# Kernel optimization log

Measured on AMD Instinct MI355X. Metric: run time of the kernel, lower is better.

## Reference

```python
import jax, jax.numpy as jnp
import numpy as np

N_NODES = 50000
N_EDGES = 800000
IN_CH = 128
HIDDEN = [128, 128]
OUT_CH = 64


def _glorot(key, shape):
    fan_in, fan_out = shape
    lim = (6.0 / (fan_in + fan_out)) ** 0.5
    return jax.random.uniform(key, shape, jnp.float32, -lim, lim)


def setup_inputs() -> dict:
    key = jax.random.key(0)
    ks = jax.random.split(key, 12)
    x = jax.random.normal(ks[0], (N_NODES, IN_CH), jnp.float32)
    edge_index = jax.random.randint(ks[1], (2, N_EDGES), 0, N_NODES, jnp.int64)
    dims = [IN_CH] + HIDDEN + [OUT_CH]
    params = {}
    for i in range(len(dims) - 1):
        d_in, d_out = dims[i], dims[i + 1]
        params[f"W_l{i}"] = _glorot(ks[2 + 3 * i], (d_in, d_out))      # neighbor weight
        params[f"W_r{i}"] = _glorot(ks[3 + 3 * i], (d_in, d_out))      # root/self weight
        params[f"b{i}"] = jnp.zeros((d_out,), jnp.float32)
    return {"x": x, "edge_index": edge_index, **params}


def _sage_conv(x, src, dst, W_l, W_r, b):
    # mean-aggregate neighbor features: messages flow src -> dst
    n = x.shape[0]
    agg = jax.ops.segment_sum(x[src], dst, num_segments=n)            # [N, d_in]
    cnt = jax.ops.segment_sum(jnp.ones((src.shape[0],), x.dtype), dst, num_segments=n)
    mean = agg / jnp.maximum(cnt, 1.0)[:, None]
    # PyG SAGEConv: lin_l(mean_neighbors) + lin_r(x_self); bias on lin_l only
    return mean @ W_l + x @ W_r + b


def reference(x, edge_index,
              W_l0, W_r0, b0,
              W_l1, W_r1, b1,
              W_l2, W_r2, b2):
    src, dst = edge_index[0], edge_index[1]
    h = _sage_conv(x, src, dst, W_l0, W_r0, b0)
    h = jax.nn.elu(h)
    h = _sage_conv(h, src, dst, W_l1, W_r1, b1)
    h = jax.nn.elu(h)
    out = _sage_conv(h, src, dst, W_l2, W_r2, b2)
    return out
```

## Files before the change

kernel.cpp:

```cpp
#include <hip/hip_runtime.h>
#include <math.h>

#define N_NODES 50000
#define N_EDGES 800000
#define IN_CH 128
#define NBUCK 196
#define BCAP 5120
#define EPB 4082

typedef unsigned short ushort_t;
typedef unsigned int uint_t;
typedef __attribute__((ext_vector_type(8))) short bf16x8;
typedef __attribute__((ext_vector_type(4))) float f32x4;

static __device__ __forceinline__ ushort_t f32_to_bf16(float f) {
    uint_t u = __float_as_uint(f);
    uint_t r = (u + 0x7fffu + ((u >> 16) & 1u)) >> 16;
    return (ushort_t)r;
}

static __device__ __forceinline__ void acc8(float* a, uint4 v) {
    a[0] += __uint_as_float(v.x << 16); a[1] += __uint_as_float(v.x & 0xffff0000u);
    a[2] += __uint_as_float(v.y << 16); a[3] += __uint_as_float(v.y & 0xffff0000u);
    a[4] += __uint_as_float(v.z << 16); a[5] += __uint_as_float(v.z & 0xffff0000u);
    a[6] += __uint_as_float(v.w << 16); a[7] += __uint_as_float(v.w & 0xffff0000u);
}

__global__ __launch_bounds__(256) void binA(
    const int* __restrict__ src, const int* __restrict__ dst,
    uint_t* __restrict__ gbcnt, uint_t* __restrict__ gbuck) {
    __shared__ uint_t hist[NBUCK];
    __shared__ uint_t excl_s[NBUCK];
    __shared__ uint_t gbase[NBUCK];
    __shared__ uint_t cur[NBUCK];
    __shared__ uint_t pfx[256];
    __shared__ uint_t stage[4096];
    __shared__ uint_t gpos[4096];
    const int t = threadIdx.x;
    const int e0 = blockIdx.x * EPB;
    const int e1 = min(e0 + EPB, N_EDGES);

    for (int i = t; i < NBUCK; i += 256) hist[i] = 0;
    __syncthreads();
    for (int e = e0 + t; e < e1; e += 256) atomicAdd(&hist[dst[e] >> 8], 1u);
    __syncthreads();
    uint_t own = (t < NBUCK) ? hist[t] : 0;
    pfx[t] = own;
    __syncthreads();
    for (int d = 1; d < 256; d <<= 1) {
        uint_t v = (t >= d) ? pfx[t - d] : 0;
        __syncthreads();
        pfx[t] += v;
        __syncthreads();
    }
    if (t < NBUCK) {
        uint_t excl = pfx[t] - own;
        excl_s[t] = excl;
        cur[t] = excl;
        gbase[t] = atomicAdd(&gbcnt[t], own);
    }
    __syncthreads();
    for (int e = e0 + t; e < e1; e += 256) {
        int d_ = dst[e];
        int b = d_ >> 8;
        uint_t p = atomicAdd(&cur[b], 1u);
        stage[p] = ((uint_t)(d_ & 255) << 16) | (uint_t)src[e];
        gpos[p] = (uint_t)b * BCAP + gbase[b] + (p - excl_s[b]);
    }
    __syncthreads();
    const int n = e1 - e0;
    for (int i = t; i < n; i += 256) gbuck[gpos[i]] = stage[i];
}

__global__ __launch_bounds__(256) void binB(
    const uint_t* __restrict__ gbcnt, const uint_t* __restrict__ gbuck,
    int* __restrict__ offs, int* __restrict__ ebuf) {
    __shared__ uint_t pairs[BCAP];
    __shared__ int stage[BCAP];
    __shared__ uint_t bscan[256];
    __shared__ uint_t h[256];
    __shared__ uint_t psc[256];
    __shared__ int cur[256];
    const int b = blockIdx.x;
    const int t = threadIdx.x;

    uint_t g = (t < NBUCK) ? gbcnt[t] : 0;
    bscan[t] = g;
    __syncthreads();
    for (int d = 1; d < 256; d <<= 1) {
        uint_t v = (t >= d) ? bscan[t - d] : 0;
        __syncthreads();
        bscan[t] += v;
        __syncthreads();
    }
    const int base = (b > 0) ? (int)bscan[b - 1] : 0;
    const uint_t n = gbcnt[b];

    for (uint_t i = t; i < n; i += 256) pairs[i] = gbuck[(size_t)b * BCAP + i];
    h[t] = 0;
    __syncthreads();
    for (uint_t i = t; i < n; i += 256) atomicAdd(&h[(pairs[i] >> 16) & 255u], 1u);
    __syncthreads();
    uint_t own = h[t];
    psc[t] = own;
    __syncthreads();
    for (int d = 1; d < 256; d <<= 1) {
        uint_t v = (t >= d) ? psc[t - d] : 0;
        __syncthreads();
        psc[t] += v;
        __syncthreads();
    }
    const int excl = (int)(psc[t] - own);
    const int node = b * 256 + t;
    if (node <= N_NODES) offs[node] = base + excl;
    cur[t] = excl;
    __syncthreads();
    for (uint_t i = t; i < n; i += 256) {
        uint_t p = pairs[i];
        int l = (p >> 16) & 255;
        int pos = atomicAdd(&cur[l], 1);
        stage[pos] = (int)(p & 0xFFFFu);
    }
    __syncthreads();
    for (uint_t i = t; i < n; i += 256) ebuf[base + (int)i] = stage[i];
}

__global__ __launch_bounds__(256) void cvt_x(const float* __restrict__ x,
                                             ushort_t* __restrict__ xb,
                                             uint_t* __restrict__ gbcnt, int n8) {
    int i = blockIdx.x * 256 + threadIdx.x;
    if (blockIdx.x == 0 && threadIdx.x < NBUCK) gbcnt[threadIdx.x] = 0;
    if (i >= n8) return;
    const float* p = x + (size_t)i * 8;
    float4 lo = *(const float4*)p;
    float4 hi = *(const float4*)(p + 4);
    bf16x8 r;
    r[0] = (short)f32_to_bf16(lo.x); r[1] = (short)f32_to_bf16(lo.y);
    r[2] = (short)f32_to_bf16(lo.z); r[3] = (short)f32_to_bf16(lo.w);
    r[4] = (short)f32_to_bf16(hi.x); r[5] = (short)f32_to_bf16(hi.y);
    r[6] = (short)f32_to_bf16(hi.z); r[7] = (short)f32_to_bf16(hi.w);
    *(bf16x8*)&xb[(size_t)i * 8] = r;
}

__global__ __launch_bounds__(256) void prep_all(
    const float* __restrict__ Wl0, const float* __restrict__ Wr0,
    const float* __restrict__ Wl1, const float* __restrict__ Wr1,
    const float* __restrict__ Wl2, const float* __restrict__ Wr2,
    ushort_t* __restrict__ Bt0, ushort_t* __restrict__ Bt1,
    ushort_t* __restrict__ Bt2) {
    int i = blockIdx.x * 256 + threadIdx.x;
    const float* Wl;
    const float* Wr;
    ushort_t* Bt;
    int C;
    if (i < 32768) {
        Wl = Wl0; Wr = Wr0; Bt = Bt0; C = 128;
    } else if (i < 65536) {
        i -= 32768; Wl = Wl1; Wr = Wr1; Bt = Bt1; C = 128;
    } else if (i < 81920) {
        i -= 65536; Wl = Wl2; Wr = Wr2; Bt = Bt2; C = 64;
    } else {
        return;
    }
    int c = i / 256, k = i % 256;
    float v = (k < 128) ? Wl[(size_t)k * C + c] : Wr[(size_t)(k - 128) * C + c];
    Bt[i] = f32_to_bf16(v);
}

__global__ __launch_bounds__(256) void gather_mean(
    const int* __restrict__ offs, const int* __restrict__ ebuf,
    const ushort_t* __restrict__ feat, ushort_t* __restrict__ M, int nNodes) {
    const int wl = threadIdx.x >> 6;
    const int lane = threadIdx.x & 63;
    const int q = lane >> 4;
    const int cl = (lane & 15) * 8;
    const int nw = gridDim.x * 4;

    for (int wid = blockIdx.x * 4 + wl; wid < nNodes; wid += nw) {
        const int o0 = offs[wid], o1 = offs[wid + 1];
        const float inv = 1.0f / fmaxf((float)(o1 - o0), 1.0f);
        float a0[8] = {0.f, 0.f, 0.f, 0.f, 0.f, 0.f, 0.f, 0.f};
        float a1[8] = {0.f, 0.f, 0.f, 0.f, 0.f, 0.f, 0.f, 0.f};
        int j = o0;
        for (; j + 8 <= o1; j += 8) {
            int s0 = ebuf[j + q];
            int s1 = ebuf[j + 4 + q];
            uint4 v0 = *(const uint4*)&feat[(size_t)s0 * 128 + cl];
            uint4 v1 = *(const uint4*)&feat[(size_t)s1 * 128 + cl];
            acc8(a0, v0);
            acc8(a1, v1);
        }
        if (j + 4 <= o1) {
            int s0 = ebuf[j + q];
            uint4 v0 = *(const uint4*)&feat[(size_t)s0 * 128 + cl];
            acc8(a0, v0);
            j += 4;
        }
        if (j + q < o1) {
            int s1 = ebuf[j + q];
            uint4 v1 = *(const uint4*)&feat[(size_t)s1 * 128 + cl];
            acc8(a1, v1);
        }
#pragma unroll
        for (int k = 0; k < 8; ++k) a0[k] += a1[k];
#pragma unroll
        for (int k = 0; k < 8; ++k) {
            a0[k] += __shfl_xor(a0[k], 16);
            a0[k] += __shfl_xor(a0[k], 32);
        }
        if (lane < 16) {
            uint4 o;
            o.x = (uint_t)f32_to_bf16(a0[0] * inv) | ((uint_t)f32_to_bf16(a0[1] * inv) << 16);
            o.y = (uint_t)f32_to_bf16(a0[2] * inv) | ((uint_t)f32_to_bf16(a0[3] * inv) << 16);
            o.z = (uint_t)f32_to_bf16(a0[4] * inv) | ((uint_t)f32_to_bf16(a0[5] * inv) << 16);
            o.w = (uint_t)f32_to_bf16(a0[6] * inv) | ((uint_t)f32_to_bf16(a0[7] * inv) << 16);
            *(uint4*)&M[(size_t)wid * 128 + cl] = o;
        }
    }
}

template <int C, bool ELU, bool OUT_F32>
__global__ __launch_bounds__(256) void gemm_fused(
    const ushort_t* __restrict__ M, const ushort_t* __restrict__ X,
    const ushort_t* __restrict__ Bt, const float* __restrict__ bias,
    void* __restrict__ out_v, int nNodes) {
    const int tid = threadIdx.x;
    const int wave = tid >> 6, lane = tid & 63;
    const int lrow = lane & 15, lgrp = lane >> 4;
    const int rowbase = blockIdx.x * 64 + (wave >> 1) * 32;
    const int colbase = blockIdx.y * 64 + (wave & 1) * 32;

    f32x4 acc[2][2] = {};

#pragma unroll
    for (int half = 0; half < 2; ++half) {
        const ushort_t* A = half ? X : M;
#pragma unroll
        for (int ks = 0; ks < 4; ++ks) {
            const int k0 = ks * 32 + lgrp * 8;
            bf16x8 a[2], bf[2];
#pragma unroll
            for (int mi = 0; mi < 2; ++mi) {
                int r = rowbase + mi * 16 + lrow;
                r = min(r, nNodes - 1);
                a[mi] = *(const bf16x8*)&A[(size_t)r * 128 + k0];
            }
#pragma unroll
            for (int ni = 0; ni < 2; ++ni) {
                int c = colbase + ni * 16 + lrow;
                bf[ni] = *(const bf16x8*)&Bt[(size_t)c * 256 + half * 128 + k0];
            }
#pragma unroll
            for (int mi = 0; mi < 2; ++mi)
#pragma unroll
                for (int ni = 0; ni < 2; ++ni)
                    acc[mi][ni] = __builtin_amdgcn_mfma_f32_16x16x32_bf16(
                        a[mi], bf[ni], acc[mi][ni], 0, 0, 0);
        }
    }

#pragma unroll
    for (int ni = 0; ni < 2; ++ni) {
        const int c = colbase + ni * 16 + lrow;
        const float bv = bias[c];
#pragma unroll
        for (int mi = 0; mi < 2; ++mi) {
#pragma unroll
            for (int j = 0; j < 4; ++j) {
                int r = rowbase + mi * 16 + lgrp * 4 + j;
                if (r >= nNodes) continue;
                float v = acc[mi][ni][j] + bv;
                if (ELU) v = v > 0.f ? v : expm1f(v);
                if (OUT_F32) ((float*)out_v)[(size_t)r * C + c] = v;
                else ((ushort_t*)out_v)[(size_t)r * C + c] = f32_to_bf16(v);
            }
        }
    }
}

extern "C" void kernel_launch(void* const* d_in, const int* in_sizes, int n_in,
                              void* d_out, int out_size, void* d_ws, size_t ws_size,
                              hipStream_t stream) {
    const float* x = (const float*)d_in[0];
    const int* ei = (const int*)d_in[1];
    const int* src = ei;
    const int* dst = ei + N_EDGES;
    const float* Wl0 = (const float*)d_in[2];
    const float* Wr0 = (const float*)d_in[3];
    const float* b0 = (const float*)d_in[4];
    const float* Wl1 = (const float*)d_in[5];
    const float* Wr1 = (const float*)d_in[6];
    const float* b1 = (const float*)d_in[7];
    const float* Wl2 = (const float*)d_in[8];
    const float* Wr2 = (const float*)d_in[9];
    const float* b2 = (const float*)d_in[10];
    float* out = (float*)d_out;

    int* wsi = (int*)d_ws;
    int* offs = wsi;
    uint_t* gbcnt = (uint_t*)(offs + 51200);
    int* ebuf = (int*)(gbcnt + 256);
    uint_t* gbuck = (uint_t*)(ebuf + 800000);
    ushort_t* Bt0 = (ushort_t*)(gbuck + NBUCK * BCAP);
    ushort_t* Bt1 = Bt0 + 128 * 256;
    ushort_t* Bt2 = Bt1 + 128 * 256;
    const long long NB = (long long)N_NODES * 128;
    ushort_t* xb = Bt2 + 64 * 256;
    ushort_t* Mb = xb + NB;
    ushort_t* hA = Mb + NB;
    ushort_t* hB = hA + NB;

    cvt_x<<<(N_NODES * 16 + 255) / 256, 256, 0, stream>>>(x, xb, gbcnt, N_NODES * 16);
    prep_all<<<(81920 + 255) / 256, 256, 0, stream>>>(
        Wl0, Wr0, Wl1, Wr1, Wl2, Wr2, Bt0, Bt1, Bt2);

    binA<<<NBUCK, 256, 0, stream>>>(src, dst, gbcnt, gbuck);
    binB<<<NBUCK, 256, 0, stream>>>(gbcnt, gbuck, offs, ebuf);

    const int GATHER_GRID = 2048;
    const int GR = (N_NODES + 63) / 64;

    gather_mean<<<GATHER_GRID, 256, 0, stream>>>(offs, ebuf, xb, Mb, N_NODES);
    gemm_fused<128, true, false><<<dim3(GR, 2), 256, 0, stream>>>(
        Mb, xb, Bt0, b0, hA, N_NODES);

    gather_mean<<<GATHER_GRID, 256, 0, stream>>>(offs, ebuf, hA, Mb, N_NODES);
    gemm_fused<128, true, false><<<dim3(GR, 2), 256, 0, stream>>>(
        Mb, hA, Bt1, b1, hB, N_NODES);

    gather_mean<<<GATHER_GRID, 256, 0, stream>>>(offs, ebuf, hB, Mb, N_NODES);
    gemm_fused<64, false, true><<<dim3(GR, 1), 256, 0, stream>>>(
        Mb, hB, Bt2, b2, out, N_NODES);
}
```

Measured before the change: 209.8 us.

## Fuse neighbor mean gather into per-layer GEMM via shared-memory tile

Each SAGE layer becomes a single kernel. A block first gathers and averages the neighbor features for its 64 nodes into an LDS tile, then runs the MFMA GEMM over the full output width, reading the mean half from LDS and the self half from global memory. This removes the intermediate mean buffer's global write and re-read and cuts the launch count from six to three. In exchange, the gather runs at one block per 64 nodes (782 blocks) instead of a 2048-block grid-stride, and each wave processes its 16 nodes one after another, which may reduce memory-level parallelism for the latency-bound gather.

```diff
diff --git a/kernel.cpp b/kernel.cpp
--- a/kernel.cpp
+++ b/kernel.cpp
@@ -167,107 +167,112 @@
     Bt[i] = f32_to_bf16(v);
 }
 
-__global__ __launch_bounds__(256) void gather_mean(
+template <int C, bool ELU, bool OUT_F32>
+__global__ __launch_bounds__(256) void sage_layer(
     const int* __restrict__ offs, const int* __restrict__ ebuf,
-    const ushort_t* __restrict__ feat, ushort_t* __restrict__ M, int nNodes) {
-    const int wl = threadIdx.x >> 6;
-    const int lane = threadIdx.x & 63;
-    const int q = lane >> 4;
-    const int cl = (lane & 15) * 8;
-    const int nw = gridDim.x * 4;
-
-    for (int wid = blockIdx.x * 4 + wl; wid < nNodes; wid += nw) {
-        const int o0 = offs[wid], o1 = offs[wid + 1];
-        const float inv = 1.0f / fmaxf((float)(o1 - o0), 1.0f);
-        float a0[8] = {0.f, 0.f, 0.f, 0.f, 0.f, 0.f, 0.f, 0.f};
-        float a1[8] = {0.f, 0.f, 0.f, 0.f, 0.f, 0.f, 0.f, 0.f};
-        int j = o0;
-        for (; j + 8 <= o1; j += 8) {
-            int s0 = ebuf[j + q];
-            int s1 = ebuf[j + 4 + q];
-            uint4 v0 = *(const uint4*)&feat[(size_t)s0 * 128 + cl];
-            uint4 v1 = *(const uint4*)&feat[(size_t)s1 * 128 + cl];
-            acc8(a0, v0);
-            acc8(a1, v1);
-        }
-        if (j + 4 <= o1) {
-            int s0 = ebuf[j + q];
-            uint4 v0 = *(const uint4*)&feat[(size_t)s0 * 128 + cl];
-            acc8(a0, v0);
-            j += 4;
-        }
-        if (j + q < o1) {
-            int s1 = ebuf[j + q];
-            uint4 v1 = *(const uint4*)&feat[(size_t)s1 * 128 + cl];
-            acc8(a1, v1);
-        }
-#pragma unroll
-        for (int k = 0; k < 8; ++k) a0[k] += a1[k];
-#pragma unroll
-        for (int k = 0; k < 8; ++k) {
-            a0[k] += __shfl_xor(a0[k], 16);
-            a0[k] += __shfl_xor(a0[k], 32);
-        }
-        if (lane < 16) {
-            uint4 o;
-            o.x = (uint_t)f32_to_bf16(a0[0] * inv) | ((uint_t)f32_to_bf16(a0[1] * inv) << 16);
-            o.y = (uint_t)f32_to_bf16(a0[2] * inv) | ((uint_t)f32_to_bf16(a0[3] * inv) << 16);
-            o.z = (uint_t)f32_to_bf16(a0[4] * inv) | ((uint_t)f32_to_bf16(a0[5] * inv) << 16);
-            o.w = (uint_t)f32_to_bf16(a0[6] * inv) | ((uint_t)f32_to_bf16(a0[7] * inv) << 16);
-            *(uint4*)&M[(size_t)wid * 128 + cl] = o;
-        }
-    }
-}
-
-template <int C, bool ELU, bool OUT_F32>
-__global__ __launch_bounds__(256) void gemm_fused(
-    const ushort_t* __restrict__ M, const ushort_t* __restrict__ X,
-    const ushort_t* __restrict__ Bt, const float* __restrict__ bias,
-    void* __restrict__ out_v, int nNodes) {
+    const ushort_t* __restrict__ X, const ushort_t* __restrict__ Bt,
+    const float* __restrict__ bias, void* __restrict__ out_v, int nNodes) {
+    __shared__ ushort_t Ms[64][136];
+    constexpr int NI = C / 32;
     const int tid = threadIdx.x;
     const int wave = tid >> 6, lane = tid & 63;
+    const int n0 = blockIdx.x * 64;
+
+    {
+        const int q = lane >> 4;
+        const int cl = (lane & 15) * 8;
+        for (int i = 0; i < 16; ++i) {
+            const int row = wave * 16 + i;
+            const int wid = n0 + row;
+            if (wid >= nNodes) break;
+            const int o0 = offs[wid], o1 = offs[wid + 1];
+            const float inv = 1.0f / fmaxf((float)(o1 - o0), 1.0f);
+            float a0[8] = {0.f, 0.f, 0.f, 0.f, 0.f, 0.f, 0.f, 0.f};
+            float a1[8] = {0.f, 0.f, 0.f, 0.f, 0.f, 0.f, 0.f, 0.f};
+            int j = o0;
+            for (; j + 8 <= o1; j += 8) {
+                int s0 = ebuf[j + q];
+                int s1 = ebuf[j + 4 + q];
+                uint4 v0 = *(const uint4*)&X[(size_t)s0 * 128 + cl];
+                uint4 v1 = *(const uint4*)&X[(size_t)s1 * 128 + cl];
+                acc8(a0, v0);
+                acc8(a1, v1);
+            }
+            if (j + 4 <= o1) {
+                int s0 = ebuf[j + q];
+                uint4 v0 = *(const uint4*)&X[(size_t)s0 * 128 + cl];
+                acc8(a0, v0);
+                j += 4;
+            }
+            if (j + q < o1) {
+                int s1 = ebuf[j + q];
+                uint4 v1 = *(const uint4*)&X[(size_t)s1 * 128 + cl];
+                acc8(a1, v1);
+            }
+#pragma unroll
+            for (int k = 0; k < 8; ++k) a0[k] += a1[k];
+#pragma unroll
+            for (int k = 0; k < 8; ++k) {
+                a0[k] += __shfl_xor(a0[k], 16);
+                a0[k] += __shfl_xor(a0[k], 32);
+            }
+            if (lane < 16) {
+                uint4 o;
+                o.x = (uint_t)f32_to_bf16(a0[0] * inv) | ((uint_t)f32_to_bf16(a0[1] * inv) << 16);
+                o.y = (uint_t)f32_to_bf16(a0[2] * inv) | ((uint_t)f32_to_bf16(a0[3] * inv) << 16);
+                o.z = (uint_t)f32_to_bf16(a0[4] * inv) | ((uint_t)f32_to_bf16(a0[5] * inv) << 16);
+                o.w = (uint_t)f32_to_bf16(a0[6] * inv) | ((uint_t)f32_to_bf16(a0[7] * inv) << 16);
+                *(uint4*)&Ms[row][cl] = o;
+            }
+        }
+    }
+    __syncthreads();
+
     const int lrow = lane & 15, lgrp = lane >> 4;
-    const int rowbase = blockIdx.x * 64 + (wave >> 1) * 32;
-    const int colbase = blockIdx.y * 64 + (wave & 1) * 32;
-
-    f32x4 acc[2][2] = {};
+    const int rloc = (wave >> 1) * 32;
+    const int colbase = (wave & 1) * (C / 2);
+
+    f32x4 acc[2][NI] = {};
 
 #pragma unroll
     for (int half = 0; half < 2; ++half) {
-        const ushort_t* A = half ? X : M;
 #pragma unroll
         for (int ks = 0; ks < 4; ++ks) {
             const int k0 = ks * 32 + lgrp * 8;
-            bf16x8 a[2], bf[2];
+            bf16x8 a[2], bf[NI];
 #pragma unroll
             for (int mi = 0; mi < 2; ++mi) {
-                int r = rowbase + mi * 16 + lrow;
-                r = min(r, nNodes - 1);
-                a[mi] = *(const bf16x8*)&A[(size_t)r * 128 + k0];
-            }
-#pragma unroll
-            for (int ni = 0; ni < 2; ++ni) {
+                if (half == 0) {
+                    a[mi] = *(const bf16x8*)&Ms[rloc + mi * 16 + lrow][k0];
+                } else {
+                    int r = n0 + rloc + mi * 16 + lrow;
+                    r = min(r, nNodes - 1);
+                    a[mi] = *(const bf16x8*)&X[(size_t)r * 128 + k0];
+                }
+            }
+#pragma unroll
+            for (int ni = 0; ni < NI; ++ni) {
                 int c = colbase + ni * 16 + lrow;
                 bf[ni] = *(const bf16x8*)&Bt[(size_t)c * 256 + half * 128 + k0];
             }
 #pragma unroll
             for (int mi = 0; mi < 2; ++mi)
 #pragma unroll
-                for (int ni = 0; ni < 2; ++ni)
+                for (int ni = 0; ni < NI; ++ni)
                     acc[mi][ni] = __builtin_amdgcn_mfma_f32_16x16x32_bf16(
                         a[mi], bf[ni], acc[mi][ni], 0, 0, 0);
         }
     }
 
 #pragma unroll
-    for (int ni = 0; ni < 2; ++ni) {
+    for (int ni = 0; ni < NI; ++ni) {
         const int c = colbase + ni * 16 + lrow;
         const float bv = bias[c];
 #pragma unroll
         for (int mi = 0; mi < 2; ++mi) {
 #pragma unroll
             for (int j = 0; j < 4; ++j) {
-                int r = rowbase + mi * 16 + lgrp * 4 + j;
+                int r = n0 + rloc + mi * 16 + lgrp * 4 + j;
                 if (r >= nNodes) continue;
                 float v = acc[mi][ni][j] + bv;
                 if (ELU) v = v > 0.f ? v : expm1f(v);
@@ -306,8 +311,7 @@
     ushort_t* Bt2 = Bt1 + 128 * 256;
     const long long NB = (long long)N_NODES * 128;
     ushort_t* xb = Bt2 + 64 * 256;
-    ushort_t* Mb = xb + NB;
-    ushort_t* hA = Mb + NB;
+    ushort_t* hA = xb + NB;
     ushort_t* hB = hA + NB;
 
     cvt_x<<<(N_NODES * 16 + 255) / 256, 256, 0, stream>>>(x, xb, gbcnt, N_NODES * 16);
@@ -317,18 +321,12 @@
     binA<<<NBUCK, 256, 0, stream>>>(src, dst, gbcnt, gbuck);
     binB<<<NBUCK, 256, 0, stream>>>(gbcnt, gbuck, offs, ebuf);
 
-    const int GATHER_GRID = 2048;
     const int GR = (N_NODES + 63) / 64;
 
-    gather_mean<<<GATHER_GRID, 256, 0, stream>>>(offs, ebuf, xb, Mb, N_NODES);
-    gemm_fused<128, true, false><<<dim3(GR, 2), 256, 0, stream>>>(
-        Mb, xb, Bt0, b0, hA, N_NODES);
-
-    gather_mean<<<GATHER_GRID, 256, 0, stream>>>(offs, ebuf, hA, Mb, N_NODES);
-    gemm_fused<128, true, false><<<dim3(GR, 2), 256, 0, stream>>>(
-        Mb, hA, Bt1, b1, hB, N_NODES);
-
-    gather_mean<<<GATHER_GRID, 256, 0, stream>>>(offs, ebuf, hB, Mb, N_NODES);
-    gemm_fused<64, false, true><<<dim3(GR, 1), 256, 0, stream>>>(
-        Mb, hB, Bt2, b2, out, N_NODES);
-}
+    sage_layer<128, true, false><<<GR, 256, 0, stream>>>(
+        offs, ebuf, xb, Bt0, b0, hA, N_NODES);
+    sage_layer<128, true, false><<<GR, 256, 0, stream>>>(
+        offs, ebuf, hA, Bt1, b1, hB, N_NODES);
+    sage_layer<64, false, true><<<GR, 256, 0, stream>>>(
+        offs, ebuf, hB, Bt2, b2, out, N_NODES);
+}
```

Result: slower. 240.0 us (+14.4%).

## Reorder last SAGE layer to transform before aggregating over 64 channels

Applied to the files above, without the earlier changes.

The final layer now multiplies node features by W_l2 and W_r2 first, using the linearity of mean aggregation. It then gathers and averages the 64-wide projected neighbor features instead of the 128-wide hidden features. This halves the bytes moved by the irregular gather in the last layer and replaces the separate gather and GEMM with a split GEMM followed by a gather that adds the root term and bias. The cost is extra workspace for the projected neighbor (bf16) and root (fp32) outputs. Rounding the neighbor projection to bf16 before averaging shifts where precision is lost.

```diff
diff --git a/kernel.cpp b/kernel.cpp
--- a/kernel.cpp
+++ b/kernel.cpp
@@ -24,6 +24,11 @@
     a[2] += __uint_as_float(v.y << 16); a[3] += __uint_as_float(v.y & 0xffff0000u);
     a[4] += __uint_as_float(v.z << 16); a[5] += __uint_as_float(v.z & 0xffff0000u);
     a[6] += __uint_as_float(v.w << 16); a[7] += __uint_as_float(v.w & 0xffff0000u);
+}
+
+static __device__ __forceinline__ void acc4(float* a, uint2 v) {
+    a[0] += __uint_as_float(v.x << 16); a[1] += __uint_as_float(v.x & 0xffff0000u);
+    a[2] += __uint_as_float(v.y << 16); a[3] += __uint_as_float(v.y & 0xffff0000u);
 }
 
 __global__ __launch_bounds__(256) void binA(
@@ -147,24 +152,23 @@
     const float* __restrict__ Wl1, const float* __restrict__ Wr1,
     const float* __restrict__ Wl2, const float* __restrict__ Wr2,
     ushort_t* __restrict__ Bt0, ushort_t* __restrict__ Bt1,
-    ushort_t* __restrict__ Bt2) {
+    ushort_t* __restrict__ Bt2s) {
     int i = blockIdx.x * 256 + threadIdx.x;
-    const float* Wl;
-    const float* Wr;
-    ushort_t* Bt;
-    int C;
     if (i < 32768) {
-        Wl = Wl0; Wr = Wr0; Bt = Bt0; C = 128;
+        int c = i / 256, k = i % 256;
+        float v = (k < 128) ? Wl0[(size_t)k * 128 + c] : Wr0[(size_t)(k - 128) * 128 + c];
+        Bt0[i] = f32_to_bf16(v);
     } else if (i < 65536) {
-        i -= 32768; Wl = Wl1; Wr = Wr1; Bt = Bt1; C = 128;
+        i -= 32768;
+        int c = i / 256, k = i % 256;
+        float v = (k < 128) ? Wl1[(size_t)k * 128 + c] : Wr1[(size_t)(k - 128) * 128 + c];
+        Bt1[i] = f32_to_bf16(v);
     } else if (i < 81920) {
-        i -= 65536; Wl = Wl2; Wr = Wr2; Bt = Bt2; C = 64;
-    } else {
-        return;
-    }
-    int c = i / 256, k = i % 256;
-    float v = (k < 128) ? Wl[(size_t)k * C + c] : Wr[(size_t)(k - 128) * C + c];
-    Bt[i] = f32_to_bf16(v);
+        i -= 65536;
+        int c = i >> 7, k = i & 127;
+        float v = (c < 64) ? Wl2[(size_t)k * 64 + c] : Wr2[(size_t)k * 64 + (c - 64)];
+        Bt2s[i] = f32_to_bf16(v);
+    }
 }
 
 __global__ __launch_bounds__(256) void gather_mean(
@@ -219,11 +223,10 @@
     }
 }
 
-template <int C, bool ELU, bool OUT_F32>
-__global__ __launch_bounds__(256) void gemm_fused(
+__global__ __launch_bounds__(256) void gemm_fused128(
     const ushort_t* __restrict__ M, const ushort_t* __restrict__ X,
     const ushort_t* __restrict__ Bt, const float* __restrict__ bias,
-    void* __restrict__ out_v, int nNodes) {
+    ushort_t* __restrict__ out_b, int nNodes) {
     const int tid = threadIdx.x;
     const int wave = tid >> 6, lane = tid & 63;
     const int lrow = lane & 15, lgrp = lane >> 4;
@@ -270,10 +273,117 @@
                 int r = rowbase + mi * 16 + lgrp * 4 + j;
                 if (r >= nNodes) continue;
                 float v = acc[mi][ni][j] + bv;
-                if (ELU) v = v > 0.f ? v : expm1f(v);
-                if (OUT_F32) ((float*)out_v)[(size_t)r * C + c] = v;
-                else ((ushort_t*)out_v)[(size_t)r * C + c] = f32_to_bf16(v);
+                v = v > 0.f ? v : expm1f(v);
+                out_b[(size_t)r * 128 + c] = f32_to_bf16(v);
             }
+        }
+    }
+}
+
+__global__ __launch_bounds__(256) void gemm_split(
+    const ushort_t* __restrict__ X, const ushort_t* __restrict__ Bt2s,
+    const float* __restrict__ bias, ushort_t* __restrict__ pl,
+    float* __restrict__ pr, int nNodes) {
+    const int tid = threadIdx.x;
+    const int wave = tid >> 6, lane = tid & 63;
+    const int lrow = lane & 15, lgrp = lane >> 4;
+    const int rowbase = blockIdx.x * 64 + (wave >> 1) * 32;
+    const int colbase = (wave & 1) * 64;
+
+    f32x4 acc[2][4] = {};
+
+#pragma unroll
+    for (int ks = 0; ks < 4; ++ks) {
+        const int k0 = ks * 32 + lgrp * 8;
+        bf16x8 a[2], bf[4];
+#pragma unroll
+        for (int mi = 0; mi < 2; ++mi) {
+            int r = rowbase + mi * 16 + lrow;
+            r = min(r, nNodes - 1);
+            a[mi] = *(const bf16x8*)&X[(size_t)r * 128 + k0];
+        }
+#pragma unroll
+        for (int ni = 0; ni < 4; ++ni) {
+            int c = colbase + ni * 16 + lrow;
+            bf[ni] = *(const bf16x8*)&Bt2s[(size_t)c * 128 + k0];
+        }
+#pragma unroll
+        for (int mi = 0; mi < 2; ++mi)
+#pragma unroll
+            for (int ni = 0; ni < 4; ++ni)
+                acc[mi][ni] = __builtin_amdgcn_mfma_f32_16x16x32_bf16(
+                    a[mi], bf[ni], acc[mi][ni], 0, 0, 0);
+    }
+
+    const bool is_pr = (wave & 1) != 0;
+#pragma unroll
+    for (int ni = 0; ni < 4; ++ni) {
+        const int c = colbase + ni * 16 + lrow;
+        const float bv = is_pr ? bias[c - 64] : 0.f;
+#pragma unroll
+        for (int mi = 0; mi < 2; ++mi) {
+#pragma unroll
+            for (int j = 0; j < 4; ++j) {
+                int r = rowbase + mi * 16 + lgrp * 4 + j;
+                if (r >= nNodes) continue;
+                float v = acc[mi][ni][j];
+                if (is_pr) pr[(size_t)r * 64 + (c - 64)] = v + bv;
+                else pl[(size_t)r * 64 + c] = f32_to_bf16(v);
+            }
+        }
+    }
+}
+
+__global__ __launch_bounds__(256) void gather64_final(
+    const int* __restrict__ offs, const int* __restrict__ ebuf,
+    const ushort_t* __restrict__ pl, const float* __restrict__ pr,
+    float* __restrict__ out, int nNodes) {
+    const int wl = threadIdx.x >> 6;
+    const int lane = threadIdx.x & 63;
+    const int q = lane >> 4;
+    const int cl = (lane & 15) * 4;
+    const int nw = gridDim.x * 4;
+
+    for (int wid = blockIdx.x * 4 + wl; wid < nNodes; wid += nw) {
+        const int o0 = offs[wid], o1 = offs[wid + 1];
+        const float inv = 1.0f / fmaxf((float)(o1 - o0), 1.0f);
+        float a0[4] = {0.f, 0.f, 0.f, 0.f};
+        float a1[4] = {0.f, 0.f, 0.f, 0.f};
+        int j = o0;
+        for (; j + 8 <= o1; j += 8) {
+            int s0 = ebuf[j + q];
+            int s1 = ebuf[j + 4 + q];
+            uint2 v0 = *(const uint2*)&pl[(size_t)s0 * 64 + cl];
+            uint2 v1 = *(const uint2*)&pl[(size_t)s1 * 64 + cl];
+            acc4(a0, v0);
+            acc4(a1, v1);
+        }
+        if (j + 4 <= o1) {
+            int s0 = ebuf[j + q];
+            uint2 v0 = *(const uint2*)&pl[(size_t)s0 * 64 + cl];
+            acc4(a0, v0);
+            j += 4;
+        }
+        if (j + q < o1) {
+            int s1 = ebuf[j + q];
+            uint2 v1 = *(const uint2*)&pl[(size_t)s1 * 64 + cl];
+            acc4(a1, v1);
+        }
+#pragma unroll
+        for (int k = 0; k < 4; ++k) a0[k] += a1[k];
+#pragma unroll
+        for (int k = 0; k < 4; ++k) {
+            a0[k] += __shfl_xor(a0[k], 16);
+            a0[k] += __shfl_xor(a0[k], 32);
+        }
+        if (lane < 16) {
+            float4 pv = *(const float4*)&pr[(size_t)wid * 64 + cl];
+            float4 o;
+            o.x = a0[0] * inv + pv.x;
+            o.y = a0[1] * inv + pv.y;
+            o.z = a0[2] * inv + pv.z;
+            o.w = a0[3] * inv + pv.w;
+            *(float4*)&out[(size_t)wid * 64 + cl] = o;
         }
     }
 }
@@ -303,16 +413,18 @@
     uint_t* gbuck = (uint_t*)(ebuf + 800000);
     ushort_t* Bt0 = (ushort_t*)(gbuck + NBUCK * BCAP);
     ushort_t* Bt1 = Bt0 + 128 * 256;
-    ushort_t* Bt2 = Bt1 + 128 * 256;
+    ushort_t* Bt2s = Bt1 + 128 * 256;
     const long long NB = (long long)N_NODES * 128;
-    ushort_t* xb = Bt2 + 64 * 256;
+    ushort_t* xb = Bt2s + 128 * 128;
     ushort_t* Mb = xb + NB;
     ushort_t* hA = Mb + NB;
     ushort_t* hB = hA + NB;
+    ushort_t* pl = hB + NB;
+    float* pr = (float*)(pl + (long long)N_NODES * 64);
 
     cvt_x<<<(N_NODES * 16 + 255) / 256, 256, 0, stream>>>(x, xb, gbcnt, N_NODES * 16);
     prep_all<<<(81920 + 255) / 256, 256, 0, stream>>>(
-        Wl0, Wr0, Wl1, Wr1, Wl2, Wr2, Bt0, Bt1, Bt2);
+        Wl0, Wr0, Wl1, Wr1, Wl2, Wr2, Bt0, Bt1, Bt2s);
 
     binA<<<NBUCK, 256, 0, stream>>>(src, dst, gbcnt, gbuck);
     binB<<<NBUCK, 256, 0, stream>>>(gbcnt, gbuck, offs, ebuf);
@@ -321,14 +433,11 @@
     const int GR = (N_NODES + 63) / 64;
 
     gather_mean<<<GATHER_GRID, 256, 0, stream>>>(offs, ebuf, xb, Mb, N_NODES);
-    gemm_fused<128, true, false><<<dim3(GR, 2), 256, 0, stream>>>(
-        Mb, xb, Bt0, b0, hA, N_NODES);
+    gemm_fused128<<<dim3(GR, 2), 256, 0, stream>>>(Mb, xb, Bt0, b0, hA, N_NODES);
 
     gather_mean<<<GATHER_GRID, 256, 0, stream>>>(offs, ebuf, hA, Mb, N_NODES);
-    gemm_fused<128, true, false><<<dim3(GR, 2), 256, 0, stream>>>(
-        Mb, hA, Bt1, b1, hB, N_NODES);
-
-    gather_mean<<<GATHER_GRID, 256, 0, stream>>>(offs, ebuf, hB, Mb, N_NODES);
-    gemm_fused<64, false, true><<<dim3(GR, 1), 256, 0, stream>>>(
-        Mb, hB, Bt2, b2, out, N_NODES);
-}
+    gemm_fused128<<<dim3(GR, 2), 256, 0, stream>>>(Mb, hA, Bt1, b1, hB, N_NODES);
+
+    gemm_split<<<GR, 256, 0, stream>>>(hB, Bt2s, b2, pl, pr, N_NODES);
+    gather64_final<<<GATHER_GRID, 256, 0, stream>>>(offs, ebuf, pl, pr, out, N_NODES);
+}
```

Result: faster. 203.9 us (-2.8%).
